# Optimization experiments

Measured on AMD Instinct MI355X. Metric: run time of the kernel, lower is better.

Reference implementation:

```python
import jax, jax.numpy as jnp
import numpy as np

LATENT_DIM = 128
KQ_DIM = 32
B, N, K = 8, 16384, 16


def setup_inputs() -> dict:
    key = jax.random.key(0)
    k1, k2, k3, k4, k5, k6 = jax.random.split(key, 6)
    features = jax.random.normal(k1, (B, N, LATENT_DIM), dtype=jnp.float32)
    ks_w = jax.random.normal(k2, (KQ_DIM, LATENT_DIM), dtype=jnp.float32) * (LATENT_DIM ** -0.5)
    ks_b = jax.random.normal(k3, (KQ_DIM,), dtype=jnp.float32) * 0.01
    qs_w = jax.random.normal(k4, (KQ_DIM, LATENT_DIM), dtype=jnp.float32) * (LATENT_DIM ** -0.5)
    qs_b = jax.random.normal(k5, (KQ_DIM,), dtype=jnp.float32) * 0.01
    indices = jax.random.randint(k6, (3, B, N, K), 0, N, dtype=jnp.int64)
    return {"features": features, "ks_w": ks_w, "ks_b": ks_b,
            "qs_w": qs_w, "qs_b": qs_b, "indices": indices}


def reference(features, ks_w, ks_b, qs_w, qs_b, indices):
    # features: [B, N, latent_dim]; indices: [3, B, N, K]
    b, n, _ = features.shape
    k = indices.shape[-1]
    # Linear projections (torch Linear: x @ W^T + b)
    flatten_ks = jnp.einsum('bnl,dl->bnd', features, ks_w) + ks_b  # [B,N,D]
    flatten_qs = jnp.einsum('bnl,dl->bnd', features, qs_w) + qs_b  # [B,N,D]
    d = flatten_ks.shape[-1]
    # gather along node dim N using index channels 1 (x) and 2 (y)
    x_idx = indices[1].reshape(b, n * k)  # [B, N*K]
    y_idx = indices[2].reshape(b, n * k)
    x_features = jnp.take_along_axis(flatten_ks, x_idx[..., None], axis=1).reshape(b, n, k, d)
    y_features = jnp.take_along_axis(flatten_qs, y_idx[..., None], axis=1).reshape(b, n, k, d)
    # scaled dot-product affinity
    logits = jnp.sum(x_features * y_features, axis=-1) * (d ** -0.5)  # [B,N,K]
    return logits
```

## Files before the change

kernel.cpp:

```cpp
#include <hip/hip_runtime.h>

#define BATCH   8
#define NNODES  16384
#define KNBR    16
#define LATENT  128
#define DOUT    32
#define NROWS   (BATCH * NNODES)

typedef __attribute__((ext_vector_type(8))) short short8;
typedef __attribute__((ext_vector_type(4))) float floatx4;

__device__ __forceinline__ unsigned short f2bf(float f) {
    unsigned u = __float_as_uint(f);
    u += 0x7fff + ((u >> 16) & 1);
    return (unsigned short)(u >> 16);
}

__device__ __forceinline__ float dot2bf(unsigned a, unsigned b) {
    float alo = __uint_as_float(a << 16);
    float ahi = __uint_as_float(a & 0xffff0000u);
    float blo = __uint_as_float(b << 16);
    float bhi = __uint_as_float(b & 0xffff0000u);
    return alo * blo + ahi * bhi;
}

#define APAD 72
#define BPAD 136

__global__ __launch_bounds__(256) void proj_kernel(
    const float* __restrict__ feats,
    const float* __restrict__ kw, const float* __restrict__ kb,
    const float* __restrict__ qw, const float* __restrict__ qb,
    unsigned short* __restrict__ tkb, unsigned short* __restrict__ tqb)
{
    __shared__ unsigned short A_lds[256 * APAD];
    __shared__ unsigned short B_lds[64 * BPAD];
    __shared__ float bias_lds[64];

    const int tid  = threadIdx.x;
    const int lane = tid & 63;
    const int w    = tid >> 6;
    const long long blk_row = (long long)blockIdx.x * 256;

    {
        const float4* kw4 = (const float4*)kw;
        const float4* qw4 = (const float4*)qw;
#pragma unroll
        for (int i = 0; i < 8; ++i) {
            const int linear = i * 256 + tid;
            const int row = linear >> 5;
            const int c4  = linear & 31;
            const float4 v = (row < 32) ? kw4[row * 32 + c4] : qw4[(row - 32) * 32 + c4];
            unsigned lo = f2bf(v.x) | ((unsigned)f2bf(v.y) << 16);
            unsigned hi = f2bf(v.z) | ((unsigned)f2bf(v.w) << 16);
            *(uint2*)&B_lds[row * BPAD + c4 * 4] = make_uint2(lo, hi);
        }
        if (tid < 64) bias_lds[tid] = (tid < 32) ? kb[tid] : qb[tid - 32];
    }

    const int m = lane & 15;
    const int q = lane >> 4;

    floatx4 acc[4][4];
#pragma unroll
    for (int rt = 0; rt < 4; ++rt)
#pragma unroll
        for (int ct = 0; ct < 4; ++ct) acc[rt][ct] = (floatx4){0.f, 0.f, 0.f, 0.f};

    const float4* f4 = (const float4*)feats;
    const int s_c4   = tid & 15;
    const int s_rowg = tid >> 4;

    for (int ch = 0; ch < 2; ++ch) {
        __syncthreads();
#pragma unroll
        for (int i = 0; i < 16; ++i) {
            const int row = i * 16 + s_rowg;
            const float4 v = f4[(blk_row + row) * 32 + ch * 16 + s_c4];
            unsigned lo = f2bf(v.x) | ((unsigned)f2bf(v.y) << 16);
            unsigned hi = f2bf(v.z) | ((unsigned)f2bf(v.w) << 16);
            *(uint2*)&A_lds[row * APAD + s_c4 * 4] = make_uint2(lo, hi);
        }
        __syncthreads();

#pragma unroll
        for (int ks = 0; ks < 2; ++ks) {
            const int kk = ks * 32 + q * 8;
            const int kg = ch * 64 + kk;
            short8 bf[4];
#pragma unroll
            for (int ct = 0; ct < 4; ++ct)
                bf[ct] = *(const short8*)&B_lds[(ct * 16 + m) * BPAD + kg];
#pragma unroll
            for (int rt = 0; rt < 4; ++rt) {
                const short8 af = *(const short8*)&A_lds[(w * 64 + rt * 16 + m) * APAD + kk];
#pragma unroll
                for (int ct = 0; ct < 4; ++ct)
                    acc[rt][ct] = __builtin_amdgcn_mfma_f32_16x16x32_bf16(af, bf[ct], acc[rt][ct], 0, 0, 0);
            }
        }
    }

#pragma unroll
    for (int rt = 0; rt < 4; ++rt) {
#pragma unroll
        for (int reg = 0; reg < 4; ++reg) {
            const long long row = blk_row + w * 64 + rt * 16 + q * 4 + reg;
#pragma unroll
            for (int ct = 0; ct < 4; ++ct) {
                const float val = acc[rt][ct][reg] + bias_lds[ct * 16 + m];
                if (ct < 2) tkb[row * DOUT + ct * 16 + m]       = f2bf(val);
                else        tqb[row * DOUT + (ct - 2) * 16 + m] = f2bf(val);
            }
        }
    }
}

__global__ __launch_bounds__(256) void gather_dot_kernel(
    const unsigned short* __restrict__ tkb, const unsigned short* __restrict__ tqb,
    const int* __restrict__ idx, float* __restrict__ out)
{
    const long long NK  = (long long)NNODES * KNBR;
    const long long BNK = NK * BATCH;

    const int b   = blockIdx.x & 7;
    const int blk = blockIdx.x >> 3;
    const int grp = threadIdx.x >> 2;
    const int j   = threadIdx.x & 3;

    const uint4* tb_k = (const uint4*)(tkb + (long long)b * NNODES * DOUT);
    const uint4* tb_q = (const uint4*)(tqb + (long long)b * NNODES * DOUT);

#pragma unroll
    for (int p = 0; p < 4; ++p) {
        const long long local = (long long)blk * 256 + p * 64 + grp;
        const long long o     = (long long)b * NK + local;

        const int xi = idx[BNK + o];
        const int yi = idx[2 * BNK + o];

        const uint4 x = tb_k[(long long)xi * 4 + j];
        const uint4 y = tb_q[(long long)yi * 4 + j];
        float s = dot2bf(x.x, y.x) + dot2bf(x.y, y.y)
                + dot2bf(x.z, y.z) + dot2bf(x.w, y.w);
        s += __shfl_xor(s, 1);
        s += __shfl_xor(s, 2);
        if (j == 0) out[o] = s * 0.17677669529663687f;
    }
}

extern "C" void kernel_launch(void* const* d_in, const int* in_sizes, int n_in,
                              void* d_out, int out_size, void* d_ws, size_t ws_size,
                              hipStream_t stream)
{
    const float* feats = (const float*)d_in[0];
    const float* kw    = (const float*)d_in[1];
    const float* kb    = (const float*)d_in[2];
    const float* qw    = (const float*)d_in[3];
    const float* qb    = (const float*)d_in[4];
    const int*   idx   = (const int*)d_in[5];
    float*       out   = (float*)d_out;

    unsigned short* tkb = (unsigned short*)d_ws;
    unsigned short* tqb = tkb + (long long)NROWS * DOUT;

    proj_kernel<<<NROWS / 256, 256, 0, stream>>>(feats, kw, kb, qw, qb, tkb, tqb);
    gather_dot_kernel<<<(int)((long long)BATCH * NNODES * KNBR / 256), 256, 0, stream>>>(
        tkb, tqb, idx, out);
}
```

Before: 150.0 us.

## Load MFMA operands directly from global memory, dropping LDS staging, add nontemporal hints

The projection kernel no longer stages features and weights through shared memory with barriers. Each lane now loads its MFMA fragments straight from global memory, converts them to bf16 in registers, and reads the bias from global. Nontemporal loads and stores are added for the streamed features, indices and outputs in both kernels. This removes LDS traffic and __syncthreads, but global accesses become strided per lane (each lane reads 32 bytes of a 512-byte row), and the weights are re-read by every wave.

```diff
diff --git a/kernel.cpp b/kernel.cpp
--- a/kernel.cpp
+++ b/kernel.cpp
@@ -9,11 +9,21 @@
 
 typedef __attribute__((ext_vector_type(8))) short short8;
 typedef __attribute__((ext_vector_type(4))) float floatx4;
+typedef __attribute__((ext_vector_type(4))) unsigned uintx4;
 
 __device__ __forceinline__ unsigned short f2bf(float f) {
     unsigned u = __float_as_uint(f);
     u += 0x7fff + ((u >> 16) & 1);
     return (unsigned short)(u >> 16);
+}
+
+__device__ __forceinline__ short8 pack8(const floatx4 a, const floatx4 b) {
+    short8 r;
+    r[0] = (short)f2bf(a.x); r[1] = (short)f2bf(a.y);
+    r[2] = (short)f2bf(a.z); r[3] = (short)f2bf(a.w);
+    r[4] = (short)f2bf(b.x); r[5] = (short)f2bf(b.y);
+    r[6] = (short)f2bf(b.z); r[7] = (short)f2bf(b.w);
+    return r;
 }
 
 __device__ __forceinline__ float dot2bf(unsigned a, unsigned b) {
@@ -24,40 +34,16 @@
     return alo * blo + ahi * bhi;
 }
 
-#define APAD 72
-#define BPAD 136
-
 __global__ __launch_bounds__(256) void proj_kernel(
     const float* __restrict__ feats,
     const float* __restrict__ kw, const float* __restrict__ kb,
     const float* __restrict__ qw, const float* __restrict__ qb,
     unsigned short* __restrict__ tkb, unsigned short* __restrict__ tqb)
 {
-    __shared__ unsigned short A_lds[256 * APAD];
-    __shared__ unsigned short B_lds[64 * BPAD];
-    __shared__ float bias_lds[64];
-
     const int tid  = threadIdx.x;
     const int lane = tid & 63;
     const int w    = tid >> 6;
     const long long blk_row = (long long)blockIdx.x * 256;
-
-    {
-        const float4* kw4 = (const float4*)kw;
-        const float4* qw4 = (const float4*)qw;
-#pragma unroll
-        for (int i = 0; i < 8; ++i) {
-            const int linear = i * 256 + tid;
-            const int row = linear >> 5;
-            const int c4  = linear & 31;
-            const float4 v = (row < 32) ? kw4[row * 32 + c4] : qw4[(row - 32) * 32 + c4];
-            unsigned lo = f2bf(v.x) | ((unsigned)f2bf(v.y) << 16);
-            unsigned hi = f2bf(v.z) | ((unsigned)f2bf(v.w) << 16);
-            *(uint2*)&B_lds[row * BPAD + c4 * 4] = make_uint2(lo, hi);
-        }
-        if (tid < 64) bias_lds[tid] = (tid < 32) ? kb[tid] : qb[tid - 32];
-    }
-
     const int m = lane & 15;
     const int q = lane >> 4;
 
@@ -67,39 +53,39 @@
 #pragma unroll
         for (int ct = 0; ct < 4; ++ct) acc[rt][ct] = (floatx4){0.f, 0.f, 0.f, 0.f};
 
-    const float4* f4 = (const float4*)feats;
-    const int s_c4   = tid & 15;
-    const int s_rowg = tid >> 4;
-
-    for (int ch = 0; ch < 2; ++ch) {
-        __syncthreads();
-#pragma unroll
-        for (int i = 0; i < 16; ++i) {
-            const int row = i * 16 + s_rowg;
-            const float4 v = f4[(blk_row + row) * 32 + ch * 16 + s_c4];
-            unsigned lo = f2bf(v.x) | ((unsigned)f2bf(v.y) << 16);
-            unsigned hi = f2bf(v.z) | ((unsigned)f2bf(v.w) << 16);
-            *(uint2*)&A_lds[row * APAD + s_c4 * 4] = make_uint2(lo, hi);
-        }
-        __syncthreads();
+    const floatx4* f4  = (const floatx4*)feats;
+    const floatx4* kw4 = (const floatx4*)kw;
+    const floatx4* qw4 = (const floatx4*)qw;
 
 #pragma unroll
-        for (int ks = 0; ks < 2; ++ks) {
-            const int kk = ks * 32 + q * 8;
-            const int kg = ch * 64 + kk;
-            short8 bf[4];
+    for (int ks = 0; ks < 4; ++ks) {
+        const int kf4 = ks * 8 + q * 2;
+
+        short8 bf[4];
+#pragma unroll
+        for (int ct = 0; ct < 4; ++ct) {
+            const floatx4* wb = (ct < 2) ? kw4 : qw4;
+            const int row = (ct & 1) * 16 + m;
+            const floatx4 b0 = wb[row * 32 + kf4];
+            const floatx4 b1 = wb[row * 32 + kf4 + 1];
+            bf[ct] = pack8(b0, b1);
+        }
+#pragma unroll
+        for (int rt = 0; rt < 4; ++rt) {
+            const long long arow = blk_row + w * 64 + rt * 16 + m;
+            const floatx4 a0 = __builtin_nontemporal_load(&f4[arow * 32 + kf4]);
+            const floatx4 a1 = __builtin_nontemporal_load(&f4[arow * 32 + kf4 + 1]);
+            const short8 af = pack8(a0, a1);
 #pragma unroll
             for (int ct = 0; ct < 4; ++ct)
-                bf[ct] = *(const short8*)&B_lds[(ct * 16 + m) * BPAD + kg];
-#pragma unroll
-            for (int rt = 0; rt < 4; ++rt) {
-                const short8 af = *(const short8*)&A_lds[(w * 64 + rt * 16 + m) * APAD + kk];
-#pragma unroll
-                for (int ct = 0; ct < 4; ++ct)
-                    acc[rt][ct] = __builtin_amdgcn_mfma_f32_16x16x32_bf16(af, bf[ct], acc[rt][ct], 0, 0, 0);
-            }
+                acc[rt][ct] = __builtin_amdgcn_mfma_f32_16x16x32_bf16(af, bf[ct], acc[rt][ct], 0, 0, 0);
         }
     }
+
+    float bias[4];
+#pragma unroll
+    for (int ct = 0; ct < 4; ++ct)
+        bias[ct] = (ct < 2) ? kb[ct * 16 + m] : qb[(ct - 2) * 16 + m];
 
 #pragma unroll
     for (int rt = 0; rt < 4; ++rt) {
@@ -108,7 +94,7 @@
             const long long row = blk_row + w * 64 + rt * 16 + q * 4 + reg;
 #pragma unroll
             for (int ct = 0; ct < 4; ++ct) {
-                const float val = acc[rt][ct][reg] + bias_lds[ct * 16 + m];
+                const float val = acc[rt][ct][reg] + bias[ct];
                 if (ct < 2) tkb[row * DOUT + ct * 16 + m]       = f2bf(val);
                 else        tqb[row * DOUT + (ct - 2) * 16 + m] = f2bf(val);
             }
@@ -128,24 +114,25 @@
     const int grp = threadIdx.x >> 2;
     const int j   = threadIdx.x & 3;
 
-    const uint4* tb_k = (const uint4*)(tkb + (long long)b * NNODES * DOUT);
-    const uint4* tb_q = (const uint4*)(tqb + (long long)b * NNODES * DOUT);
+    const uintx4* tb_k = (const uintx4*)(tkb + (long long)b * NNODES * DOUT);
+    const uintx4* tb_q = (const uintx4*)(tqb + (long long)b * NNODES * DOUT);
 
 #pragma unroll
     for (int p = 0; p < 4; ++p) {
         const long long local = (long long)blk * 256 + p * 64 + grp;
         const long long o     = (long long)b * NK + local;
 
-        const int xi = idx[BNK + o];
-        const int yi = idx[2 * BNK + o];
+        const int xi = __builtin_nontemporal_load(&idx[BNK + o]);
+        const int yi = __builtin_nontemporal_load(&idx[2 * BNK + o]);
 
-        const uint4 x = tb_k[(long long)xi * 4 + j];
-        const uint4 y = tb_q[(long long)yi * 4 + j];
+        const uintx4 x = tb_k[(long long)xi * 4 + j];
+        const uintx4 y = tb_q[(long long)yi * 4 + j];
         float s = dot2bf(x.x, y.x) + dot2bf(x.y, y.y)
                 + dot2bf(x.z, y.z) + dot2bf(x.w, y.w);
         s += __shfl_xor(s, 1);
         s += __shfl_xor(s, 2);
-        if (j == 0) out[o] = s * 0.17677669529663687f;
+        if (j == 0)
+            __builtin_nontemporal_store(s * 0.17677669529663687f, &out[o]);
     }
 }
 
```

Measured after the change: 160.0 us. 6.7% more time.
